# Kernel optimization log

Measured on AMD Instinct MI355X. Metric: run time of the kernel, lower is better.

The kernel has to match this reference:

```python
import jax, jax.numpy as jnp
import numpy as np

B, S, D, H = 2, 2048, 1024, 16
HD = D // H  # head dim = 64


def setup_inputs() -> dict:
    key = jax.random.key(0)
    ks = jax.random.split(key, 5)
    scale = 1.0 / np.sqrt(D)
    return {
        "hidden_states": jax.random.normal(ks[0], (B, S, D), jnp.float32),
        "attention_mask": jax.random.normal(ks[1], (B, 1, 1, S), jnp.float32),
        "Wq": jax.random.normal(ks[2], (D, D), jnp.float32) * scale,
        "bq": jnp.zeros((D,), jnp.float32),
        "Wk": jax.random.normal(ks[3], (D, D), jnp.float32) * scale,
        "bk": jnp.zeros((D,), jnp.float32),
        "Wv": jax.random.normal(ks[4], (D, D), jnp.float32) * scale,
        "bv": jnp.zeros((D,), jnp.float32),
    }


def _split_heads(x):
    # [B,S,D] -> [B,H,S,HD]
    return x.reshape(B, S, H, HD).transpose(0, 2, 1, 3)


def reference(hidden_states, attention_mask, Wq, bq, Wk, bk, Wv, bv):
    # torch Linear: y = x @ W.T + b
    q = _split_heads(hidden_states @ Wq.T + bq)
    k = _split_heads(hidden_states @ Wk.T + bk)
    v = _split_heads(hidden_states @ Wv.T + bv)

    scores = jnp.einsum("bhqd,bhkd->bhqk", q, k)
    # Faithful to source: with a mask present, the 1/sqrt(head_dim) scaling
    # is overwritten and raw scores are multiplied by the binary key mask.
    mask = (attention_mask >= 0).astype(scores.dtype)  # [B,1,1,S]
    probs = scores * mask
    # dropout prob = 0 (eval) -> identity

    ctx = jnp.einsum("bhqk,bhkd->bhqd", probs, v)
    ctx = ctx.transpose(0, 2, 1, 3).reshape(B, S, D)
    return ctx
```

## Files before the change

kernel.cpp:

```cpp
#include <hip/hip_runtime.h>

#define BB 2
#define SS 2048
#define DD 1024
#define HH 16
#define HDIM 64
#define MTOT 4096

typedef unsigned short u16;
typedef __bf16 bf16_t;
typedef bf16_t bf16x8 __attribute__((ext_vector_type(8)));
typedef float floatx4 __attribute__((ext_vector_type(4)));

__device__ __forceinline__ float bf2f(u16 u) {
  union { unsigned int i; float f; } x;
  x.i = ((unsigned int)u) << 16;
  return x.f;
}
__device__ __forceinline__ u16 f2bf(float f) {
  union { float f; unsigned int i; } x;
  x.f = f;
  unsigned int r = x.i + 0x7fffu + ((x.i >> 16) & 1u);
  return (u16)(r >> 16);
}

__device__ __forceinline__ void gload16(const u16* g, u16* l) {
  __builtin_amdgcn_global_load_lds(
      (const __attribute__((address_space(1))) unsigned int*)g,
      (__attribute__((address_space(3))) unsigned int*)l, 16, 0, 0);
}

__global__ __launch_bounds__(256) void cast_to_bf16(
    const float* __restrict__ hs, const float* __restrict__ wq,
    const float* __restrict__ wk, const float* __restrict__ wv,
    u16* __restrict__ hs_b, u16* __restrict__ wq_b,
    u16* __restrict__ wk_b, u16* __restrict__ wv_b,
    float* __restrict__ mfull) {
  int fid = blockIdx.x * 256 + threadIdx.x;
  if (fid >= 1835008) {
    int z = fid - 1835008;
    float4 zero = {0.f, 0.f, 0.f, 0.f};
    reinterpret_cast<float4*>(mfull)[z] = zero;
    return;
  }
  const float* src;
  u16* dst;
  int local;
  if (fid < 1048576) { src = hs; dst = hs_b; local = fid; }
  else if (fid < 1310720) { src = wq; dst = wq_b; local = fid - 1048576; }
  else if (fid < 1572864) { src = wk; dst = wk_b; local = fid - 1310720; }
  else { src = wv; dst = wv_b; local = fid - 1572864; }
  float4 v = reinterpret_cast<const float4*>(src)[local];
  ushort4 o;
  o.x = f2bf(v.x); o.y = f2bf(v.y); o.z = f2bf(v.z); o.w = f2bf(v.w);
  reinterpret_cast<ushort4*>(dst)[local] = o;
}

#define BKK 32
__global__ __launch_bounds__(256) void qkv_gemm_kernel(
    const u16* __restrict__ A,
    const u16* __restrict__ Wq, const u16* __restrict__ Wk, const u16* __restrict__ Wv,
    const float* __restrict__ bq, const float* __restrict__ bk, const float* __restrict__ bv,
    u16* __restrict__ Qo, u16* __restrict__ Ko, u16* __restrict__ Vo) {
  __shared__ u16 sA[128 * BKK];
  __shared__ u16 sB[128 * BKK];
  const int mt = blockIdx.y, ntall = blockIdx.x;
  const int seg = ntall >> 3, nt = ntall & 7;
  const u16* Wp = (seg == 0) ? Wq : (seg == 1) ? Wk : Wv;
  const float* bp = (seg == 0) ? bq : (seg == 1) ? bk : bv;
  u16* Out = (seg == 0) ? Qo : (seg == 1) ? Ko : Vo;
  const int m0 = mt * 128, n0 = nt * 128;
  const int tid = threadIdx.x;
  const int lane = tid & 63, wave = tid >> 6;
  const int wm = (wave >> 1) * 64, wn = (wave & 1) * 64;
  const int quad = lane >> 4, l16 = lane & 15;
  const int srow0 = wave * 32 + (lane >> 2);
  const int scol = (lane & 3) * 8;
  floatx4 acc[4][4] = {};
  for (int k0 = 0; k0 < DD; k0 += BKK) {
#pragma unroll
    for (int c = 0; c < 2; ++c) {
      int r = srow0 + c * 16;
      gload16(A + (size_t)(m0 + r) * DD + k0 + scol, sA + r * BKK + scol);
      gload16(Wp + (size_t)(n0 + r) * DD + k0 + scol, sB + r * BKK + scol);
    }
    __syncthreads();
    bf16x8 af[4], bfr[4];
#pragma unroll
    for (int i = 0; i < 4; ++i) {
      af[i]  = *reinterpret_cast<const bf16x8*>(sA + (wm + i * 16 + l16) * BKK + quad * 8);
      bfr[i] = *reinterpret_cast<const bf16x8*>(sB + (wn + i * 16 + l16) * BKK + quad * 8);
    }
#pragma unroll
    for (int i = 0; i < 4; ++i)
#pragma unroll
      for (int j = 0; j < 4; ++j)
        acc[i][j] = __builtin_amdgcn_mfma_f32_16x16x32_bf16(af[i], bfr[j], acc[i][j], 0, 0, 0);
    __syncthreads();
  }
#pragma unroll
  for (int j = 0; j < 4; ++j) {
    int col = n0 + wn + j * 16 + l16;
    float bias = bp[col];
#pragma unroll
    for (int i = 0; i < 4; ++i) {
#pragma unroll
      for (int r = 0; r < 4; ++r) {
        int row = m0 + wm + i * 16 + quad * 4 + r;
        Out[(size_t)row * DD + col] = f2bf(acc[i][j][r] + bias);
      }
    }
  }
}

__global__ __launch_bounds__(256) void m_partial_kernel(
    const u16* __restrict__ Kb, const u16* __restrict__ Vb,
    const float* __restrict__ am, float* __restrict__ mfull) {
  __shared__ float sK[64 * 68];
  __shared__ float sV[64 * 68];
  const int bh = blockIdx.y;
  const int b = bh >> 4, h = bh & 15;
  const int tid = threadIdx.x;
  const int e0 = (tid & 15) * 4, d0 = (tid >> 4) * 4;
  float acc[4][4] = {};
  for (int cs = 0; cs < 2; ++cs) {
    const int s0 = (blockIdx.x * 2 + cs) * 64;
    if (cs) __syncthreads();
#pragma unroll
    for (int c = 0; c < 2; ++c) {
      int L = tid + c * 256;
      int srow = L >> 3;
      int col = (L & 7) * 8;
      size_t g = (size_t)(b * SS + s0 + srow) * DD + h * HDIM + col;
      uint4 kraw = *reinterpret_cast<const uint4*>(Kb + g);
      uint4 vraw = *reinterpret_cast<const uint4*>(Vb + g);
      float m = (am[b * SS + s0 + srow] >= 0.f) ? 1.f : 0.f;
      unsigned int kw[4] = {kraw.x, kraw.y, kraw.z, kraw.w};
      unsigned int vw[4] = {vraw.x, vraw.y, vraw.z, vraw.w};
#pragma unroll
      for (int q = 0; q < 4; ++q) {
        sK[srow * 68 + col + 2 * q]     = m * bf2f((u16)(kw[q] & 0xffffu));
        sK[srow * 68 + col + 2 * q + 1] = m * bf2f((u16)(kw[q] >> 16));
        sV[srow * 68 + col + 2 * q]     = bf2f((u16)(vw[q] & 0xffffu));
        sV[srow * 68 + col + 2 * q + 1] = bf2f((u16)(vw[q] >> 16));
      }
    }
    __syncthreads();
    for (int s = 0; s < 64; ++s) {
      float4 kk = *reinterpret_cast<const float4*>(&sK[s * 68 + e0]);
      float4 vv = *reinterpret_cast<const float4*>(&sV[s * 68 + d0]);
      float ka[4] = {kk.x, kk.y, kk.z, kk.w};
      float va[4] = {vv.x, vv.y, vv.z, vv.w};
#pragma unroll
      for (int i = 0; i < 4; ++i)
#pragma unroll
        for (int j = 0; j < 4; ++j) acc[i][j] += ka[i] * va[j];
    }
  }
  float* outp = mfull + (size_t)bh * 4096;
#pragma unroll
  for (int i = 0; i < 4; ++i)
#pragma unroll
    for (int j = 0; j < 4; ++j)
      atomicAdd(&outp[(e0 + i) * 64 + d0 + j], acc[i][j]);
}

__global__ __launch_bounds__(256) void ctx_kernel(
    const u16* __restrict__ Qb, const float* __restrict__ M, float* __restrict__ Out) {
  __shared__ float sM[64 * 68];
  __shared__ float sQ[64 * 68];
  const int mchunk = blockIdx.x;
  const int h = blockIdx.y;
  const int m0 = mchunk * 64;
  const int b = m0 >> 11;
  const int bh = b * HH + h;
  const int tid = threadIdx.x;
  const float* Mp = M + (size_t)bh * 4096;
#pragma unroll
  for (int c = 0; c < 16; ++c) {
    int L = c * 256 + tid;
    int e = L >> 6, d = L & 63;
    sM[e * 68 + d] = Mp[L];
  }
#pragma unroll
  for (int c = 0; c < 2; ++c) {
    int L = tid + c * 256;
    int row = L >> 3, col = (L & 7) * 8;
    uint4 q = *reinterpret_cast<const uint4*>(Qb + (size_t)(m0 + row) * DD + h * HDIM + col);
    unsigned int w[4] = {q.x, q.y, q.z, q.w};
#pragma unroll
    for (int t = 0; t < 4; ++t) {
      sQ[row * 68 + col + 2 * t]     = bf2f((u16)(w[t] & 0xffffu));
      sQ[row * 68 + col + 2 * t + 1] = bf2f((u16)(w[t] >> 16));
    }
  }
  __syncthreads();
  const int d0 = (tid & 15) * 4, ml0 = (tid >> 4) * 4;
  float acc[4][4] = {};
  for (int e4 = 0; e4 < 64; e4 += 4) {
    float4 mm[4], qq[4];
#pragma unroll
    for (int t = 0; t < 4; ++t)
      mm[t] = *reinterpret_cast<const float4*>(&sM[(e4 + t) * 68 + d0]);
#pragma unroll
    for (int i = 0; i < 4; ++i)
      qq[i] = *reinterpret_cast<const float4*>(&sQ[(ml0 + i) * 68 + e4]);
    float ma[4][4], qa[4][4];
#pragma unroll
    for (int t = 0; t < 4; ++t) {
      ma[t][0] = mm[t].x; ma[t][1] = mm[t].y; ma[t][2] = mm[t].z; ma[t][3] = mm[t].w;
      qa[t][0] = qq[t].x; qa[t][1] = qq[t].y; qa[t][2] = qq[t].z; qa[t][3] = qq[t].w;
    }
#pragma unroll
    for (int i = 0; i < 4; ++i)
#pragma unroll
      for (int t = 0; t < 4; ++t)
#pragma unroll
        for (int j = 0; j < 4; ++j)
          acc[i][j] += qa[i][t] * ma[t][j];
  }
#pragma unroll
  for (int i = 0; i < 4; ++i) {
    float4 o = {acc[i][0], acc[i][1], acc[i][2], acc[i][3]};
    *reinterpret_cast<float4*>(Out + (size_t)(m0 + ml0 + i) * DD + h * HDIM + d0) = o;
  }
}

extern "C" void kernel_launch(void* const* d_in, const int* in_sizes, int n_in,
                              void* d_out, int out_size, void* d_ws, size_t ws_size,
                              hipStream_t stream) {
  const float* hs = (const float*)d_in[0];
  const float* am = (const float*)d_in[1];
  const float* wq = (const float*)d_in[2];
  const float* bq = (const float*)d_in[3];
  const float* wk = (const float*)d_in[4];
  const float* bk = (const float*)d_in[5];
  const float* wv = (const float*)d_in[6];
  const float* bv = (const float*)d_in[7];
  float* out = (float*)d_out;
  char* ws = (char*)d_ws;

  u16* hs_b = (u16*)(ws);
  u16* wq_b = (u16*)(ws + 8388608);
  u16* wk_b = (u16*)(ws + 10485760);
  u16* wv_b = (u16*)(ws + 12582912);
  u16* q_b  = (u16*)(ws + 14680064);
  u16* k_b  = (u16*)(ws + 23068672);
  u16* v_b  = (u16*)(ws + 31457280);
  float* mfull = (float*)(ws + 39845888);

  cast_to_bf16<<<7296, 256, 0, stream>>>(hs, wq, wk, wv, hs_b, wq_b, wk_b, wv_b, mfull);
  qkv_gemm_kernel<<<dim3(24, 32), 256, 0, stream>>>(hs_b, wq_b, wk_b, wv_b,
                                                    bq, bk, bv, q_b, k_b, v_b);
  m_partial_kernel<<<dim3(16, 32), 256, 0, stream>>>(k_b, v_b, am, mfull);
  ctx_kernel<<<dim3(64, 16), 256, 0, stream>>>(q_b, mfull, out);
}
```

Baseline: 163.2 us.

## Use 32x32 MFMA in QKV GEMM and replace atomic K^T V reduction with partials

Switches the QKV projection GEMM from 16x16x32 to 32x32x16 bf16 MFMA tiles with a 2x2 accumulator layout per wave, which needs fewer LDS fragment loads per MFMA. Separately, the K^T V partial kernel now covers four sequence chunks per block and writes per-block partial matrices with plain float4 stores instead of atomicAdd. The context kernel sums the 8 partials while loading them. This also drops the zero-initialisation of the accumulator buffer from the cast kernel, at the cost of extra partial reads in the context kernel and fewer blocks for the partial stage.

```diff
diff --git a/kernel.cpp b/kernel.cpp
--- a/kernel.cpp
+++ b/kernel.cpp
@@ -11,6 +11,7 @@
 typedef __bf16 bf16_t;
 typedef bf16_t bf16x8 __attribute__((ext_vector_type(8)));
 typedef float floatx4 __attribute__((ext_vector_type(4)));
+typedef float floatx16 __attribute__((ext_vector_type(16)));
 
 __device__ __forceinline__ float bf2f(u16 u) {
   union { unsigned int i; float f; } x;
@@ -34,15 +35,8 @@
     const float* __restrict__ hs, const float* __restrict__ wq,
     const float* __restrict__ wk, const float* __restrict__ wv,
     u16* __restrict__ hs_b, u16* __restrict__ wq_b,
-    u16* __restrict__ wk_b, u16* __restrict__ wv_b,
-    float* __restrict__ mfull) {
+    u16* __restrict__ wk_b, u16* __restrict__ wv_b) {
   int fid = blockIdx.x * 256 + threadIdx.x;
-  if (fid >= 1835008) {
-    int z = fid - 1835008;
-    float4 zero = {0.f, 0.f, 0.f, 0.f};
-    reinterpret_cast<float4*>(mfull)[z] = zero;
-    return;
-  }
   const float* src;
   u16* dst;
   int local;
@@ -73,10 +67,10 @@
   const int tid = threadIdx.x;
   const int lane = tid & 63, wave = tid >> 6;
   const int wm = (wave >> 1) * 64, wn = (wave & 1) * 64;
-  const int quad = lane >> 4, l16 = lane & 15;
+  const int l32 = lane & 31, khalf = lane >> 5;
   const int srow0 = wave * 32 + (lane >> 2);
   const int scol = (lane & 3) * 8;
-  floatx4 acc[4][4] = {};
+  floatx16 acc[2][2] = {};
   for (int k0 = 0; k0 < DD; k0 += BKK) {
 #pragma unroll
     for (int c = 0; c < 2; ++c) {
@@ -85,29 +79,33 @@
       gload16(Wp + (size_t)(n0 + r) * DD + k0 + scol, sB + r * BKK + scol);
     }
     __syncthreads();
-    bf16x8 af[4], bfr[4];
-#pragma unroll
-    for (int i = 0; i < 4; ++i) {
-      af[i]  = *reinterpret_cast<const bf16x8*>(sA + (wm + i * 16 + l16) * BKK + quad * 8);
-      bfr[i] = *reinterpret_cast<const bf16x8*>(sB + (wn + i * 16 + l16) * BKK + quad * 8);
-    }
-#pragma unroll
-    for (int i = 0; i < 4; ++i)
-#pragma unroll
-      for (int j = 0; j < 4; ++j)
-        acc[i][j] = __builtin_amdgcn_mfma_f32_16x16x32_bf16(af[i], bfr[j], acc[i][j], 0, 0, 0);
+#pragma unroll
+    for (int kk = 0; kk < 2; ++kk) {
+      bf16x8 af[2], bfr[2];
+#pragma unroll
+      for (int i = 0; i < 2; ++i)
+        af[i] = *reinterpret_cast<const bf16x8*>(sA + (wm + i * 32 + l32) * BKK + kk * 16 + khalf * 8);
+#pragma unroll
+      for (int j = 0; j < 2; ++j)
+        bfr[j] = *reinterpret_cast<const bf16x8*>(sB + (wn + j * 32 + l32) * BKK + kk * 16 + khalf * 8);
+#pragma unroll
+      for (int i = 0; i < 2; ++i)
+#pragma unroll
+        for (int j = 0; j < 2; ++j)
+          acc[i][j] = __builtin_amdgcn_mfma_f32_32x32x16_bf16(af[i], bfr[j], acc[i][j], 0, 0, 0);
+    }
     __syncthreads();
   }
 #pragma unroll
-  for (int j = 0; j < 4; ++j) {
-    int col = n0 + wn + j * 16 + l16;
+  for (int j = 0; j < 2; ++j) {
+    int col = n0 + wn + j * 32 + l32;
     float bias = bp[col];
 #pragma unroll
-    for (int i = 0; i < 4; ++i) {
-#pragma unroll
-      for (int r = 0; r < 4; ++r) {
-        int row = m0 + wm + i * 16 + quad * 4 + r;
-        Out[(size_t)row * DD + col] = f2bf(acc[i][j][r] + bias);
+    for (int i = 0; i < 2; ++i) {
+#pragma unroll
+      for (int reg = 0; reg < 16; ++reg) {
+        int row = m0 + wm + i * 32 + (reg & 3) + 8 * (reg >> 2) + 4 * khalf;
+        Out[(size_t)row * DD + col] = f2bf(acc[i][j][reg] + bias);
       }
     }
   }
@@ -115,7 +113,7 @@
 
 __global__ __launch_bounds__(256) void m_partial_kernel(
     const u16* __restrict__ Kb, const u16* __restrict__ Vb,
-    const float* __restrict__ am, float* __restrict__ mfull) {
+    const float* __restrict__ am, float* __restrict__ mpart) {
   __shared__ float sK[64 * 68];
   __shared__ float sV[64 * 68];
   const int bh = blockIdx.y;
@@ -123,8 +121,8 @@
   const int tid = threadIdx.x;
   const int e0 = (tid & 15) * 4, d0 = (tid >> 4) * 4;
   float acc[4][4] = {};
-  for (int cs = 0; cs < 2; ++cs) {
-    const int s0 = (blockIdx.x * 2 + cs) * 64;
+  for (int cs = 0; cs < 4; ++cs) {
+    const int s0 = (blockIdx.x * 4 + cs) * 64;
     if (cs) __syncthreads();
 #pragma unroll
     for (int c = 0; c < 2; ++c) {
@@ -157,16 +155,16 @@
         for (int j = 0; j < 4; ++j) acc[i][j] += ka[i] * va[j];
     }
   }
-  float* outp = mfull + (size_t)bh * 4096;
-#pragma unroll
-  for (int i = 0; i < 4; ++i)
-#pragma unroll
-    for (int j = 0; j < 4; ++j)
-      atomicAdd(&outp[(e0 + i) * 64 + d0 + j], acc[i][j]);
+  float* outp = mpart + ((size_t)(blockIdx.x * 32 + bh)) * 4096;
+#pragma unroll
+  for (int i = 0; i < 4; ++i) {
+    float4 o = {acc[i][0], acc[i][1], acc[i][2], acc[i][3]};
+    *reinterpret_cast<float4*>(&outp[(e0 + i) * 64 + d0]) = o;
+  }
 }
 
 __global__ __launch_bounds__(256) void ctx_kernel(
-    const u16* __restrict__ Qb, const float* __restrict__ M, float* __restrict__ Out) {
+    const u16* __restrict__ Qb, const float* __restrict__ mpart, float* __restrict__ Out) {
   __shared__ float sM[64 * 68];
   __shared__ float sQ[64 * 68];
   const int mchunk = blockIdx.x;
@@ -175,12 +173,18 @@
   const int b = m0 >> 11;
   const int bh = b * HH + h;
   const int tid = threadIdx.x;
-  const float* Mp = M + (size_t)bh * 4096;
-#pragma unroll
-  for (int c = 0; c < 16; ++c) {
-    int L = c * 256 + tid;
-    int e = L >> 6, d = L & 63;
-    sM[e * 68 + d] = Mp[L];
+#pragma unroll
+  for (int c = 0; c < 4; ++c) {
+    int L4 = c * 256 + tid;
+    float4 s = {0.f, 0.f, 0.f, 0.f};
+#pragma unroll
+    for (int pc = 0; pc < 8; ++pc) {
+      const float4* p4 = reinterpret_cast<const float4*>(mpart + ((size_t)(pc * 32 + bh)) * 4096);
+      float4 t = p4[L4];
+      s.x += t.x; s.y += t.y; s.z += t.z; s.w += t.w;
+    }
+    int e = L4 >> 4, d = (L4 & 15) * 4;
+    *reinterpret_cast<float4*>(&sM[e * 68 + d]) = s;
   }
 #pragma unroll
   for (int c = 0; c < 2; ++c) {
@@ -247,11 +251,11 @@
   u16* q_b  = (u16*)(ws + 14680064);
   u16* k_b  = (u16*)(ws + 23068672);
   u16* v_b  = (u16*)(ws + 31457280);
-  float* mfull = (float*)(ws + 39845888);
-
-  cast_to_bf16<<<7296, 256, 0, stream>>>(hs, wq, wk, wv, hs_b, wq_b, wk_b, wv_b, mfull);
+  float* mpart = (float*)(ws + 39845888);
+
+  cast_to_bf16<<<7168, 256, 0, stream>>>(hs, wq, wk, wv, hs_b, wq_b, wk_b, wv_b);
   qkv_gemm_kernel<<<dim3(24, 32), 256, 0, stream>>>(hs_b, wq_b, wk_b, wv_b,
                                                     bq, bk, bv, q_b, k_b, v_b);
-  m_partial_kernel<<<dim3(16, 32), 256, 0, stream>>>(k_b, v_b, am, mfull);
-  ctx_kernel<<<dim3(64, 16), 256, 0, stream>>>(q_b, mfull, out);
-}
+  m_partial_kernel<<<dim3(8, 32), 256, 0, stream>>>(k_b, v_b, am, mpart);
+  ctx_kernel<<<dim3(64, 16), 256, 0, stream>>>(q_b, mpart, out);
+}
```

Result: faster. 153.4 us (-6.0%).
